# Kernel optimization log

Hardware: AMD Instinct MI355X
Metric: run time of the kernel (lower is better)

## Reference

```python
import jax, jax.numpy as jnp
import numpy as np
import math

B, S, H = 4, 4096, 64
WINDOW = 2


def setup_inputs() -> dict:
    key = jax.random.key(0)
    ks = jax.random.split(key, 7)
    s = 0.05
    return {
        "feature": jax.random.normal(ks[0], (B, S, H), dtype=jnp.float32),
        "Wq": jax.random.normal(ks[1], (H, H), dtype=jnp.float32) * s,
        "bq": jax.random.normal(ks[2], (H,), dtype=jnp.float32) * s,
        "Wk": jax.random.normal(ks[3], (H, H), dtype=jnp.float32) * s,
        "bk": jax.random.normal(ks[4], (H,), dtype=jnp.float32) * s,
        "Wv": jax.random.normal(ks[5], (H, H), dtype=jnp.float32) * s,
        "bv": jax.random.normal(ks[6], (H,), dtype=jnp.float32) * s,
    }


def reference(feature, Wq, bq, Wk, bk, Wv, bv):
    b, seq, d_k = feature.shape
    # torch nn.Linear: y = x @ W.T + b
    q = feature @ Wq.T + bq  # [B,S,H]
    k = feature @ Wk.T + bk
    v = feature @ Wv.T + bv

    # banded 0/1 mask, |i-j| <= window, then softmax over the FULL row
    # (faithful to the original: zeros outside the band also get exp(0)=1 weight)
    idx = jnp.arange(seq)
    band = (jnp.abs(idx[:, None] - idx[None, :]) <= WINDOW).astype(jnp.float32)  # [S,S]
    weights = jax.nn.softmax(band, axis=-1)  # [S,S]

    # locally-averaged K: weights @ k, shared across batch
    mixed_k = jnp.einsum('st,bth->bsh', weights, k)  # [B,S,H]
    scores = jnp.einsum('bsh,bth->bst', q, mixed_k) / math.sqrt(d_k)  # [B,S,S]
    attn = jax.nn.softmax(scores, axis=-1)
    out = jnp.einsum('bst,bth->bsh', attn, v)  # [B,S,H]
    return out
```

## Files before the change

### kernel.cpp

```cpp
#include <hip/hip_runtime.h>
#include <hip/hip_bf16.h>
#include <math.h>

#define SEQ 4096
#define HD  64
#define NBATCH 4

#define EM1   1.71828182845904523536f
#define INVD5 (1.0f/(4096.f + 5.f*EM1))
#define INVD4 (1.0f/(4096.f + 4.f*EM1))
#define INVD3 (1.0f/(4096.f + 3.f*EM1))

typedef __attribute__((ext_vector_type(8))) short short8;
typedef __attribute__((ext_vector_type(4))) float f32x4;

__device__ __forceinline__ f32x4 mfma16(short8 a, short8 b, f32x4 c) {
    return __builtin_amdgcn_mfma_f32_16x16x32_bf16(a, b, c, 0, 0, 0);
}

__device__ __forceinline__ short bfs(float x) {
    __hip_bfloat16 h = __float2bfloat16(x);
    return *(short*)&h;
}

__device__ __forceinline__ short8 pack8(float4 a, float4 b) {
    short8 r;
    r[0] = bfs(a.x); r[1] = bfs(a.y); r[2] = bfs(a.z); r[3] = bfs(a.w);
    r[4] = bfs(b.x); r[5] = bfs(b.y); r[6] = bfs(b.z); r[7] = bfs(b.w);
    return r;
}

__device__ __forceinline__ float blo(unsigned v) { return __uint_as_float(v << 16); }
__device__ __forceinline__ float bhi(unsigned v) { return __uint_as_float(v & 0xffff0000u); }
__device__ __forceinline__ float b2f(__hip_bfloat16 h) { return __bfloat162float(h); }

__global__ __launch_bounds__(256) void wpack_kernel(
    const float* __restrict__ Wq, const float* __restrict__ Wk,
    const float* __restrict__ Wv, __hip_bfloat16* __restrict__ Wb)
{
    const int m = blockIdx.x, tid = threadIdx.x;
    const float* W = (m == 0) ? Wq : (m == 1) ? Wk : Wv;
    const float s = (m == 0) ? 0.125f : 1.f;
    const float* src = W + tid * 16;
    float4 a0 = *(const float4*)(src);
    float4 a1 = *(const float4*)(src + 4);
    float4 a2 = *(const float4*)(src + 8);
    float4 a3 = *(const float4*)(src + 12);
    a0.x*=s; a0.y*=s; a0.z*=s; a0.w*=s;
    a1.x*=s; a1.y*=s; a1.z*=s; a1.w*=s;
    a2.x*=s; a2.y*=s; a2.z*=s; a2.w*=s;
    a3.x*=s; a3.y*=s; a3.z*=s; a3.w*=s;
    __hip_bfloat16* dst = Wb + m * 4096 + tid * 16;
    *(short8*)(dst)     = pack8(a0, a1);
    *(short8*)(dst + 8) = pack8(a2, a3);
}

__global__ __launch_bounds__(128) void proj_kernel(
    const float* __restrict__ feat, const __hip_bfloat16* __restrict__ Wb,
    const float* __restrict__ bq, const float* __restrict__ bk,
    const float* __restrict__ bv,
    __hip_bfloat16* __restrict__ qsb, __hip_bfloat16* __restrict__ ktb,
    __hip_bfloat16* __restrict__ vtb,
    float* __restrict__ kpart, float* __restrict__ vpart)
{
    __shared__ __hip_bfloat16 tscr[64 * 72];
    __shared__ float kred[2][64];

    const int tid  = threadIdx.x;
    const int wave = tid >> 6, lane = tid & 63;
    const int quad = lane >> 4, ln = lane & 15;
    const int R0 = blockIdx.x * 32;
    const int b  = R0 >> 12;
    const int t0 = R0 & (SEQ - 1);

    short8 af0, af1;
    {
        const float* fp = feat + (size_t)(R0 + wave * 16 + ln) * HD + quad * 8;
        af0 = pack8(*(const float4*)(fp),      *(const float4*)(fp + 4));
        af1 = pack8(*(const float4*)(fp + 32), *(const float4*)(fp + 36));
    }

    const float* Bs[3] = {bq, bk, bv};

    #pragma unroll
    for (int m = 0; m < 3; ++m) {
        const __hip_bfloat16* W = Wb + m * 4096;
        const float* bias = Bs[m];
        #pragma unroll
        for (int ct = 0; ct < 4; ++ct) {
            const int col = ct * 16 + ln;
            const __hip_bfloat16* wp = W + col * 64 + quad * 8;
            short8 b0 = *(const short8*)(wp);
            short8 b1 = *(const short8*)(wp + 32);
            f32x4 c = {};
            c = mfma16(af0, b0, c);
            c = mfma16(af1, b1, c);

            if (m == 0) {
                const float bl = bias[col] * 0.125f;
                #pragma unroll
                for (int r = 0; r < 4; ++r)
                    qsb[(size_t)(R0 + wave * 16 + quad * 4 + r) * HD + col] =
                        __float2bfloat16(c[r] + bl);
            } else {
                const float bl = bias[col];
                float tot = c[0] + c[1] + c[2] + c[3];
                tot += __shfl_xor(tot, 16);
                tot += __shfl_xor(tot, 32);
                if (quad == 0) kred[wave][col] = tot;
                #pragma unroll
                for (int r = 0; r < 4; ++r)
                    tscr[col * 72 + wave * 16 + quad * 4 + r] =
                        __float2bfloat16(c[r] + bl);
            }
        }
        if (m > 0) {
            __syncthreads();
            if (tid < 64)
                ((m == 1) ? kpart : vpart)[(size_t)blockIdx.x * 64 + tid] =
                    kred[0][tid] + kred[1][tid] + 32.f * bias[tid];
            __hip_bfloat16* dst = (m == 1) ? ktb : vtb;
            #pragma unroll
            for (int i = 0; i < 2; ++i) {
                const int tsk = i * 128 + tid;
                const int hh = tsk >> 2, c8 = tsk & 3;
                short8 vv = *(const short8*)&tscr[hh * 72 + c8 * 8];
                *(short8*)(dst + ((size_t)(b * HD + hh)) * SEQ + t0 + c8 * 8) = vv;
            }
            __syncthreads();
        }
    }
}

__global__ __launch_bounds__(256) void mkernel(
    const __hip_bfloat16* __restrict__ ktb, const __hip_bfloat16* __restrict__ vtb,
    const float* __restrict__ kpart, const float* __restrict__ vpart,
    __hip_bfloat16* __restrict__ Mpart, float* __restrict__ Mcorr,
    __hip_bfloat16* __restrict__ MT, float* __restrict__ Vtot)
{
    __shared__ float vws[64 * 38];
    __shared__ __hip_bfloat16 lvt[64 * 40];
    __shared__ float scr[4][64];
    __shared__ float ktl[64], vtl[64];
    __shared__ float lc[4][64], vv_e[4][64];

    const int tid = threadIdx.x;

    if (blockIdx.y == 4) {
        if (blockIdx.x >= 16) return;
        const int b = blockIdx.x >> 2, slab = blockIdx.x & 3;
        const int h = tid & 63, g = tid >> 6;

        if (slab == 0 || slab == 3) {
            float kp = 0.f;
            for (int j = 0; j < 32; ++j)
                kp += kpart[(size_t)(b * 128 + g * 32 + j) * 64 + h];
            scr[g][h] = kp;
            __syncthreads();
            if (tid < 64) ktl[tid] = scr[0][tid] + scr[1][tid] + scr[2][tid] + scr[3][tid];
        }
        if (slab == 0) {
            __syncthreads();
            if (tid < 64) {
                const int hh = tid;
                const float kt = ktl[hh];
                const __hip_bfloat16* kr = ktb + (size_t)(b * 64 + hh) * SEQ;
                const float e0 = b2f(kr[0]), e1 = b2f(kr[1]), e2 = b2f(kr[2]), e3 = b2f(kr[3]);
                const float f0 = b2f(kr[SEQ-4]), f1 = b2f(kr[SEQ-3]);
                const float f2 = b2f(kr[SEQ-2]), f3 = b2f(kr[SEQ-1]);
                const float Sint = 5.f*kt - 4.f*e0 - 3.f*e1 - 2.f*e2 - e3
                                 - f0 - 2.f*f1 - 3.f*f2 - 4.f*f3;
                const float SlocD = Sint * INVD5
                                  + (e0+e1+e2 + f1+f2+f3) * INVD3
                                  + (e0+e1+e2+e3 + f0+f1+f2+f3) * INVD4;
                const float mktot = kt * (4092.f*INVD5 + 2.f*INVD4 + 2.f*INVD3) + EM1 * SlocD;
                MT[(size_t)b * 5120 + 64 * 64 + hh] = __float2bfloat16(mktot);
            }
        } else if (slab == 1) {
            float vp = 0.f;
            for (int j = 0; j < 32; ++j)
                vp += vpart[(size_t)(b * 128 + g * 32 + j) * 64 + h];
            scr[g][h] = vp;
            __syncthreads();
            if (tid < 64)
                Vtot[b * 64 + tid] = scr[0][tid] + scr[1][tid] + scr[2][tid] + scr[3][tid];
        } else if (slab == 2) {
            for (int i = tid; i < 15 * 64; i += 256)
                MT[(size_t)b * 5120 + 65 * 64 + i] = __float2bfloat16(0.f);
        } else {
            __syncthreads();
            {
                float vp = 0.f;
                for (int j = 0; j < 32; ++j)
                    vp += vpart[(size_t)(b * 128 + g * 32 + j) * 64 + h];
                scr[g][h] = vp;
            }
            __syncthreads();
            if (tid < 64) vtl[tid] = scr[0][tid] + scr[1][tid] + scr[2][tid] + scr[3][tid];
            if (tid < 64) {
                const int hh = tid;
                const __hip_bfloat16* kr = ktb + (size_t)(b * 64 + hh) * SEQ;
                const float e0 = b2f(kr[0]), e1 = b2f(kr[1]), e2 = b2f(kr[2]), e3 = b2f(kr[3]);
                const float f0 = b2f(kr[SEQ-4]), f1 = b2f(kr[SEQ-3]);
                const float f2 = b2f(kr[SEQ-2]), f3 = b2f(kr[SEQ-1]);
                lc[0][hh] = e0 + e1 + e2;
                lc[1][hh] = e0 + e1 + e2 + e3;
                lc[2][hh] = f0 + f1 + f2 + f3;
                lc[3][hh] = f1 + f2 + f3;
                const __hip_bfloat16* vr = vtb + (size_t)(b * 64 + hh) * SEQ;
                vv_e[0][hh] = b2f(vr[0]);
                vv_e[1][hh] = b2f(vr[1]);
                vv_e[2][hh] = b2f(vr[SEQ-2]);
                vv_e[3][hh] = b2f(vr[SEQ-1]);
            }
            __syncthreads();
            const float dd3 = INVD3 - INVD5, dd4 = INVD4 - INVD5;
            const int h1 = tid >> 2;
            const float l0 = lc[0][h1], l1 = lc[1][h1], l2 = lc[2][h1], l3 = lc[3][h1];
            const float kt1 = ktl[h1];
            #pragma unroll
            for (int j = 0; j < 16; ++j) {
                const int h2 = (tid & 3) * 16 + j;
                const float VD = INVD5 * vtl[h2]
                               + dd3 * (vv_e[0][h2] + vv_e[3][h2])
                               + dd4 * (vv_e[1][h2] + vv_e[2][h2]);
                Mcorr[(size_t)(b * 64 + h1) * 64 + h2] =
                    EM1 * (dd3 * (l0 * vv_e[0][h2] + l3 * vv_e[3][h2])
                         + dd4 * (l1 * vv_e[1][h2] + l2 * vv_e[2][h2]))
                    + kt1 * VD;
            }
        }
        return;
    }

    const int b = blockIdx.y, chunk = blockIdx.x;
    const int t0 = chunk * 32;

    for (int i = tid; i < 64 * 18; i += 256) {
        const int r = i / 18, c = i - r * 18;
        const int gt = t0 - 2 + c * 2;
        unsigned val = 0;
        if (gt >= 0 && gt <= SEQ - 2)
            val = *(const unsigned*)(vtb + (size_t)(b * 64 + r) * SEQ + gt);
        vws[r * 38 + c * 2]     = blo(val);
        vws[r * 38 + c * 2 + 1] = bhi(val);
    }
    __syncthreads();

    {
        const int h = tid & 63, g = tid >> 6;
        float w[12];
        #pragma unroll
        for (int j = 0; j < 12; ++j) w[j] = vws[h * 38 + g * 8 + j];
        short8 o;
        #pragma unroll
        for (int i = 0; i < 8; ++i)
            o[i] = bfs(w[i] + w[i+1] + w[i+2] + w[i+3] + w[i+4]);
        *(short8*)&lvt[h * 40 + g * 8] = o;
    }
    __syncthreads();

    const int wave = tid >> 6, lane = tid & 63, quad = lane >> 4, ln = lane & 15;
    short8 a = *(const short8*)(ktb + (size_t)(b * 64 + wave * 16 + ln) * SEQ
                                + t0 + quad * 8);
    f32x4 acc[4] = {};
    #pragma unroll
    for (int ct = 0; ct < 4; ++ct) {
        short8 bb = *(const short8*)&lvt[(ct * 16 + ln) * 40 + quad * 8];
        acc[ct] = mfma16(a, bb, acc[ct]);
    }
    __hip_bfloat16* mp = Mpart + (size_t)(b * 128 + chunk) * 4096;
    #pragma unroll
    for (int ct = 0; ct < 4; ++ct)
        #pragma unroll
        for (int r = 0; r < 4; ++r)
            mp[(wave * 16 + quad * 4 + r) * 64 + ct * 16 + ln] =
                __float2bfloat16(acc[ct][r]);
}

__global__ __launch_bounds__(256) void mreduce_kernel(
    const __hip_bfloat16* __restrict__ Mpart, const float* __restrict__ Mcorr,
    __hip_bfloat16* __restrict__ MT)
{
    __shared__ float red[4][64];
    const int b = blockIdx.y, h1 = blockIdx.x;
    const int tid = threadIdx.x;
    const int g = tid >> 6, h2 = tid & 63;

    float s = 0.f;
    for (int c = g * 32; c < g * 32 + 32; ++c)
        s += b2f(Mpart[(size_t)(b * 128 + c) * 4096 + h1 * 64 + h2]);
    red[g][h2] = s;
    __syncthreads();
    if (tid < 64) {
        const float m = (EM1 * INVD5) * (red[0][tid] + red[1][tid] + red[2][tid] + red[3][tid])
                      + Mcorr[(size_t)(b * 64 + h1) * 64 + tid];
        MT[(size_t)b * 5120 + tid * 64 + h1] = __float2bfloat16(m);
    }
}

__global__ __launch_bounds__(64) void out_kernel(
    const __hip_bfloat16* __restrict__ qsb, const __hip_bfloat16* __restrict__ MT,
    const float* __restrict__ Vtot, float* __restrict__ out)
{
    const int tid = threadIdx.x;
    const int quad = tid >> 4, ln = tid & 15;
    const int R0 = blockIdx.x * 16;
    const int b = R0 >> 12;

    short8 qa0, qa1;
    {
        const __hip_bfloat16* qp = qsb + (size_t)(R0 + ln) * HD + quad * 8;
        qa0 = *(const short8*)qp;
        qa1 = *(const short8*)(qp + 32);
    }

    const __hip_bfloat16* mtb = MT + (size_t)b * 5120;
    f32x4 acc[5] = {};
    #pragma unroll
    for (int ct = 0; ct < 5; ++ct) {
        short8 b0 = *(const short8*)(mtb + (ct * 16 + ln) * 64 + quad * 8);
        short8 b1 = *(const short8*)(mtb + (ct * 16 + ln) * 64 + 32 + quad * 8);
        acc[ct] = mfma16(qa0, b0, acc[ct]);
        acc[ct] = mfma16(qa1, b1, acc[ct]);
    }

    float vt[4];
    #pragma unroll
    for (int ct = 0; ct < 4; ++ct) vt[ct] = Vtot[b * 64 + ct * 16 + ln];

    float inv[4];
    #pragma unroll
    for (int r = 0; r < 4; ++r) {
        const float den = __shfl(acc[4][r], tid & 48);
        inv[r] = 1.f / (4096.f + den);
    }
    #pragma unroll
    for (int ct = 0; ct < 4; ++ct)
        #pragma unroll
        for (int r = 0; r < 4; ++r)
            out[(size_t)(R0 + quad * 4 + r) * HD + ct * 16 + ln] =
                (vt[ct] + acc[ct][r]) * inv[r];
}

extern "C" void kernel_launch(void* const* d_in, const int* in_sizes, int n_in,
                              void* d_out, int out_size, void* d_ws, size_t ws_size,
                              hipStream_t stream)
{
    const float* feat = (const float*)d_in[0];
    const float* Wq = (const float*)d_in[1];
    const float* bq = (const float*)d_in[2];
    const float* Wk = (const float*)d_in[3];
    const float* bk = (const float*)d_in[4];
    const float* Wv = (const float*)d_in[5];
    const float* bv = (const float*)d_in[6];
    float* out = (float*)d_out;

    char* ws = (char*)d_ws;
    __hip_bfloat16* qsb   = (__hip_bfloat16*)(ws + 0);
    __hip_bfloat16* ktb   = (__hip_bfloat16*)(ws + (2u << 20));
    __hip_bfloat16* vtb   = (__hip_bfloat16*)(ws + (4u << 20));
    float*          kpart = (float*)(ws + (6u << 20));
    float*          vpart = (float*)(ws + (6u << 20) + 262144);
    __hip_bfloat16* Mpart = (__hip_bfloat16*)(ws + (6u << 20) + 524288);
    float*          Mcorr = (float*)(ws + (10u << 20) + 524288);
    __hip_bfloat16* MT    = (__hip_bfloat16*)(ws + (10u << 20) + 589824);
    float*          Vtot  = (float*)(ws + (10u << 20) + 630784);
    __hip_bfloat16* Wb    = (__hip_bfloat16*)(ws + (10u << 20) + 631808);

    wpack_kernel<<<dim3(3), dim3(256), 0, stream>>>(Wq, Wk, Wv, Wb);
    proj_kernel<<<dim3(512), dim3(128), 0, stream>>>(
        feat, Wb, bq, bk, bv, qsb, ktb, vtb, kpart, vpart);
    mkernel<<<dim3(128, 5), dim3(256), 0, stream>>>(
        ktb, vtb, kpart, vpart, Mpart, Mcorr, MT, Vtot);
    mreduce_kernel<<<dim3(64, NBATCH), dim3(256), 0, stream>>>(Mpart, Mcorr, MT);
    out_kernel<<<dim3(1024), dim3(64), 0, stream>>>(qsb, MT, Vtot, out);
}
```

Measured before the change: 88.45 us.

## Replace partial M buffers and reduce kernel with float atomics fused into output

The per-chunk bf16 M partials and the separate mreduce kernel are removed. mkernel now atomically accumulates fp32 results into a zeroed per-batch M matrix, which wpack_kernel clears. out_kernel builds the transposed, scaled M tile in shared memory per block and computes the denominator with its own MFMA. This saves one launch and the round trip of the partial buffer, at the cost of atomic contention (128 chunks per batch hitting the same 4096 addresses) and redundant M staging in each output block.

```diff
diff --git a/kernel.cpp b/kernel.cpp
--- a/kernel.cpp
+++ b/kernel.cpp
@@ -36,11 +36,17 @@
 
 __global__ __launch_bounds__(256) void wpack_kernel(
     const float* __restrict__ Wq, const float* __restrict__ Wk,
-    const float* __restrict__ Wv, __hip_bfloat16* __restrict__ Wb)
-{
-    const int m = blockIdx.x, tid = threadIdx.x;
-    const float* W = (m == 0) ? Wq : (m == 1) ? Wk : Wv;
-    const float s = (m == 0) ? 0.125f : 1.f;
+    const float* __restrict__ Wv, __hip_bfloat16* __restrict__ Wb,
+    float* __restrict__ Mfull)
+{
+    const int blk = blockIdx.x, tid = threadIdx.x;
+    if (blk >= 3) {
+        float4 z = make_float4(0.f, 0.f, 0.f, 0.f);
+        *(float4*)&Mfull[(blk - 3) * 1024 + tid * 4] = z;
+        return;
+    }
+    const float* W = (blk == 0) ? Wq : (blk == 1) ? Wk : Wv;
+    const float s = (blk == 0) ? 0.125f : 1.f;
     const float* src = W + tid * 16;
     float4 a0 = *(const float4*)(src);
     float4 a1 = *(const float4*)(src + 4);
@@ -50,7 +56,7 @@
     a1.x*=s; a1.y*=s; a1.z*=s; a1.w*=s;
     a2.x*=s; a2.y*=s; a2.z*=s; a2.w*=s;
     a3.x*=s; a3.y*=s; a3.z*=s; a3.w*=s;
-    __hip_bfloat16* dst = Wb + m * 4096 + tid * 16;
+    __hip_bfloat16* dst = Wb + blk * 4096 + tid * 16;
     *(short8*)(dst)     = pack8(a0, a1);
     *(short8*)(dst + 8) = pack8(a2, a3);
 }
@@ -135,8 +141,8 @@
 __global__ __launch_bounds__(256) void mkernel(
     const __hip_bfloat16* __restrict__ ktb, const __hip_bfloat16* __restrict__ vtb,
     const float* __restrict__ kpart, const float* __restrict__ vpart,
-    __hip_bfloat16* __restrict__ Mpart, float* __restrict__ Mcorr,
-    __hip_bfloat16* __restrict__ MT, float* __restrict__ Vtot)
+    float* __restrict__ Mfull, float* __restrict__ Mcorr,
+    float* __restrict__ mktotF, float* __restrict__ Vtot)
 {
     __shared__ float vws[64 * 38];
     __shared__ __hip_bfloat16 lvt[64 * 40];
@@ -149,6 +155,7 @@
     if (blockIdx.y == 4) {
         if (blockIdx.x >= 16) return;
         const int b = blockIdx.x >> 2, slab = blockIdx.x & 3;
+        if (slab == 2) return;
         const int h = tid & 63, g = tid >> 6;
 
         if (slab == 0 || slab == 3) {
@@ -173,8 +180,8 @@
                 const float SlocD = Sint * INVD5
                                   + (e0+e1+e2 + f1+f2+f3) * INVD3
                                   + (e0+e1+e2+e3 + f0+f1+f2+f3) * INVD4;
-                const float mktot = kt * (4092.f*INVD5 + 2.f*INVD4 + 2.f*INVD3) + EM1 * SlocD;
-                MT[(size_t)b * 5120 + 64 * 64 + hh] = __float2bfloat16(mktot);
+                mktotF[b * 64 + hh] =
+                    kt * (4092.f*INVD5 + 2.f*INVD4 + 2.f*INVD3) + EM1 * SlocD;
             }
         } else if (slab == 1) {
             float vp = 0.f;
@@ -184,9 +191,6 @@
             __syncthreads();
             if (tid < 64)
                 Vtot[b * 64 + tid] = scr[0][tid] + scr[1][tid] + scr[2][tid] + scr[3][tid];
-        } else if (slab == 2) {
-            for (int i = tid; i < 15 * 64; i += 256)
-                MT[(size_t)b * 5120 + 65 * 64 + i] = __float2bfloat16(0.f);
         } else {
             __syncthreads();
             {
@@ -269,61 +273,66 @@
         short8 bb = *(const short8*)&lvt[(ct * 16 + ln) * 40 + quad * 8];
         acc[ct] = mfma16(a, bb, acc[ct]);
     }
-    __hip_bfloat16* mp = Mpart + (size_t)(b * 128 + chunk) * 4096;
+    float* mf = Mfull + b * 4096;
     #pragma unroll
     for (int ct = 0; ct < 4; ++ct)
         #pragma unroll
         for (int r = 0; r < 4; ++r)
-            mp[(wave * 16 + quad * 4 + r) * 64 + ct * 16 + ln] =
-                __float2bfloat16(acc[ct][r]);
-}
-
-__global__ __launch_bounds__(256) void mreduce_kernel(
-    const __hip_bfloat16* __restrict__ Mpart, const float* __restrict__ Mcorr,
-    __hip_bfloat16* __restrict__ MT)
-{
-    __shared__ float red[4][64];
-    const int b = blockIdx.y, h1 = blockIdx.x;
-    const int tid = threadIdx.x;
-    const int g = tid >> 6, h2 = tid & 63;
-
-    float s = 0.f;
-    for (int c = g * 32; c < g * 32 + 32; ++c)
-        s += b2f(Mpart[(size_t)(b * 128 + c) * 4096 + h1 * 64 + h2]);
-    red[g][h2] = s;
+            atomicAdd(&mf[(wave * 16 + quad * 4 + r) * 64 + ct * 16 + ln],
+                      acc[ct][r]);
+}
+
+__global__ __launch_bounds__(256) void out_kernel(
+    const __hip_bfloat16* __restrict__ qsb, const float* __restrict__ Mfull,
+    const float* __restrict__ Mcorr, const float* __restrict__ mktotF,
+    const float* __restrict__ Vtot, float* __restrict__ out)
+{
+    __shared__ __hip_bfloat16 tscr[64 * 72];
+
+    const int tid  = threadIdx.x;
+    const int wave = tid >> 6, lane = tid & 63;
+    const int quad = lane >> 4, ln = lane & 15;
+    const int R0 = blockIdx.x * 64;
+    const int b  = R0 >> 12;
+
+    {
+        const int h2 = tid & 63, seg = tid >> 6;
+        #pragma unroll
+        for (int j = 0; j < 16; ++j) {
+            const int h1 = seg * 16 + j;
+            const float m = (EM1 * INVD5) * Mfull[b * 4096 + h1 * 64 + h2]
+                          + Mcorr[(size_t)(b * 64 + h1) * 64 + h2];
+            tscr[h2 * 72 + h1] = __float2bfloat16(m);
+        }
+    }
     __syncthreads();
-    if (tid < 64) {
-        const float m = (EM1 * INVD5) * (red[0][tid] + red[1][tid] + red[2][tid] + red[3][tid])
-                      + Mcorr[(size_t)(b * 64 + h1) * 64 + tid];
-        MT[(size_t)b * 5120 + tid * 64 + h1] = __float2bfloat16(m);
-    }
-}
-
-__global__ __launch_bounds__(64) void out_kernel(
-    const __hip_bfloat16* __restrict__ qsb, const __hip_bfloat16* __restrict__ MT,
-    const float* __restrict__ Vtot, float* __restrict__ out)
-{
-    const int tid = threadIdx.x;
-    const int quad = tid >> 4, ln = tid & 15;
-    const int R0 = blockIdx.x * 16;
-    const int b = R0 >> 12;
 
     short8 qa0, qa1;
     {
-        const __hip_bfloat16* qp = qsb + (size_t)(R0 + ln) * HD + quad * 8;
+        const __hip_bfloat16* qp = qsb + (size_t)(R0 + wave * 16 + ln) * HD + quad * 8;
         qa0 = *(const short8*)qp;
         qa1 = *(const short8*)(qp + 32);
     }
-
-    const __hip_bfloat16* mtb = MT + (size_t)b * 5120;
-    f32x4 acc[5] = {};
-    #pragma unroll
-    for (int ct = 0; ct < 5; ++ct) {
-        short8 b0 = *(const short8*)(mtb + (ct * 16 + ln) * 64 + quad * 8);
-        short8 b1 = *(const short8*)(mtb + (ct * 16 + ln) * 64 + 32 + quad * 8);
-        acc[ct] = mfma16(qa0, b0, acc[ct]);
-        acc[ct] = mfma16(qa1, b1, acc[ct]);
-    }
+    short8 mk0, mk1;
+    #pragma unroll
+    for (int j = 0; j < 8; ++j) {
+        mk0[j] = bfs(mktotF[b * 64 + quad * 8 + j]);
+        mk1[j] = bfs(mktotF[b * 64 + 32 + quad * 8 + j]);
+    }
+
+    f32x4 acc[4];
+    #pragma unroll
+    for (int ct = 0; ct < 4; ++ct) {
+        short8 b0 = *(const short8*)&tscr[(ct * 16 + ln) * 72 + quad * 8];
+        short8 b1 = *(const short8*)&tscr[(ct * 16 + ln) * 72 + 32 + quad * 8];
+        f32x4 c = {};
+        c = mfma16(qa0, b0, c);
+        c = mfma16(qa1, b1, c);
+        acc[ct] = c;
+    }
+    f32x4 accd = {};
+    accd = mfma16(qa0, mk0, accd);
+    accd = mfma16(qa1, mk1, accd);
 
     float vt[4];
     #pragma unroll
@@ -331,15 +340,13 @@
 
     float inv[4];
     #pragma unroll
-    for (int r = 0; r < 4; ++r) {
-        const float den = __shfl(acc[4][r], tid & 48);
-        inv[r] = 1.f / (4096.f + den);
-    }
+    for (int r = 0; r < 4; ++r) inv[r] = 1.f / (4096.f + accd[r]);
+
     #pragma unroll
     for (int ct = 0; ct < 4; ++ct)
         #pragma unroll
         for (int r = 0; r < 4; ++r)
-            out[(size_t)(R0 + quad * 4 + r) * HD + ct * 16 + ln] =
+            out[(size_t)(R0 + wave * 16 + quad * 4 + r) * HD + ct * 16 + ln] =
                 (vt[ct] + acc[ct][r]) * inv[r];
 }
 
@@ -357,22 +364,22 @@
     float* out = (float*)d_out;
 
     char* ws = (char*)d_ws;
-    __hip_bfloat16* qsb   = (__hip_bfloat16*)(ws + 0);
-    __hip_bfloat16* ktb   = (__hip_bfloat16*)(ws + (2u << 20));
-    __hip_bfloat16* vtb   = (__hip_bfloat16*)(ws + (4u << 20));
-    float*          kpart = (float*)(ws + (6u << 20));
-    float*          vpart = (float*)(ws + (6u << 20) + 262144);
-    __hip_bfloat16* Mpart = (__hip_bfloat16*)(ws + (6u << 20) + 524288);
-    float*          Mcorr = (float*)(ws + (10u << 20) + 524288);
-    __hip_bfloat16* MT    = (__hip_bfloat16*)(ws + (10u << 20) + 589824);
-    float*          Vtot  = (float*)(ws + (10u << 20) + 630784);
-    __hip_bfloat16* Wb    = (__hip_bfloat16*)(ws + (10u << 20) + 631808);
-
-    wpack_kernel<<<dim3(3), dim3(256), 0, stream>>>(Wq, Wk, Wv, Wb);
+    __hip_bfloat16* qsb    = (__hip_bfloat16*)(ws + 0);
+    __hip_bfloat16* ktb    = (__hip_bfloat16*)(ws + (2u << 20));
+    __hip_bfloat16* vtb    = (__hip_bfloat16*)(ws + (4u << 20));
+    float*          kpart  = (float*)(ws + (6u << 20));
+    float*          vpart  = (float*)(ws + (6u << 20) + 131072);
+    float*          Mfull  = (float*)(ws + (6u << 20) + 262144);
+    float*          Mcorr  = (float*)(ws + (6u << 20) + 327680);
+    float*          mktotF = (float*)(ws + (6u << 20) + 393216);
+    float*          Vtot   = (float*)(ws + (6u << 20) + 394240);
+    __hip_bfloat16* Wb     = (__hip_bfloat16*)(ws + (6u << 20) + 395264);
+
+    wpack_kernel<<<dim3(19), dim3(256), 0, stream>>>(Wq, Wk, Wv, Wb, Mfull);
     proj_kernel<<<dim3(512), dim3(128), 0, stream>>>(
         feat, Wb, bq, bk, bv, qsb, ktb, vtb, kpart, vpart);
     mkernel<<<dim3(128, 5), dim3(256), 0, stream>>>(
-        ktb, vtb, kpart, vpart, Mpart, Mcorr, MT, Vtot);
-    mreduce_kernel<<<dim3(64, NBATCH), dim3(256), 0, stream>>>(Mpart, Mcorr, MT);
-    out_kernel<<<dim3(1024), dim3(64), 0, stream>>>(qsb, MT, Vtot, out);
-}
+        ktb, vtb, kpart, vpart, Mfull, Mcorr, mktotF, Vtot);
+    out_kernel<<<dim3(256), dim3(256), 0, stream>>>(
+        qsb, Mfull, Mcorr, mktotF, Vtot, out);
+}
```

New measurement: 91.88 us. 1.04x slower.
